# Performance work log

Measured on AMD Instinct MI355X. Metric: run time of the kernel, lower is better.

## Reference

```python
import jax, jax.numpy as jnp
import numpy as np

N = 50000        # nodes
E = 800000       # edges
R = 8            # relations
G = 64           # g_dim
H1 = 64          # h1_dim
H2 = 32          # h2_dim (per-head for transformer, output for sage)
HEADS = 4
EPS = 1e-5       # BatchNorm eps


def setup_inputs() -> dict:
    key = jax.random.key(0)
    ks = jax.random.split(key, 16)
    def rn(k, shape, scale=0.05):
        return jax.random.normal(k, shape, dtype=jnp.float32) * scale
    return {
        "node_features": jax.random.normal(ks[0], (N, G), dtype=jnp.float32),
        "node_type": jax.random.randint(ks[1], (N,), 0, 3),
        "edge_index": jax.random.randint(ks[2], (2, E), 0, N),
        "edge_type": jax.random.randint(ks[3], (E,), 0, R),
        # RGCNConv params (per-relation weight + root weight + bias)
        "rgcn_w": rn(ks[4], (R, G, H1)),
        "rgcn_root": rn(ks[5], (G, H1)),
        "rgcn_bias": jnp.zeros((H1,), jnp.float32),
        "bn1_g": jnp.ones((H1,), jnp.float32),
        "bn1_b": jnp.zeros((H1,), jnp.float32),
        # TransformerConv params (q/k/v projections + skip)
        "wq": rn(ks[6], (H1, HEADS * H2)), "bq": jnp.zeros((HEADS * H2,), jnp.float32),
        "wk": rn(ks[7], (H1, HEADS * H2)), "bk": jnp.zeros((HEADS * H2,), jnp.float32),
        "wv": rn(ks[8], (H1, HEADS * H2)), "bv": jnp.zeros((HEADS * H2,), jnp.float32),
        "wskip": rn(ks[9], (H1, HEADS * H2)), "bskip": jnp.zeros((HEADS * H2,), jnp.float32),
        "bn2_g": jnp.ones((HEADS * H2,), jnp.float32),
        "bn2_b": jnp.zeros((HEADS * H2,), jnp.float32),
        # SAGEConv params (lin_l on aggregated neighbors has bias; lin_r on root has none)
        "sage_wl": rn(ks[10], (HEADS * H2, H2)), "sage_bl": jnp.zeros((H2,), jnp.float32),
        "sage_wr": rn(ks[11], (HEADS * H2, H2)),
        "bn3_g": jnp.ones((H2,), jnp.float32),
        "bn3_b": jnp.zeros((H2,), jnp.float32),
    }


def _bn(x, g, b):
    # BatchNorm1d in training mode: biased batch statistics over nodes
    m = x.mean(0)
    v = x.var(0)
    return g * (x - m) * jax.lax.rsqrt(v + EPS) + b


def _match(res, d):
    # F.pad(res, (0, d - c)): pads with zeros if d > c, truncates if d < c
    c = res.shape[1]
    if d > c:
        return jnp.pad(res, ((0, 0), (0, d - c)))
    return res[:, :d]


def _forward(node_features, rgcn_w, rgcn_root, rgcn_bias, bn1_g, bn1_b,
             wq, bq, wk, bk, wv, bv, wskip, bskip, bn2_g, bn2_b,
             sage_wl, sage_bl, sage_wr, bn3_g, bn3_b,
             edge_index, edge_type):
    src, dst = edge_index[0], edge_index[1]
    x = node_features
    residual = x

    # ---- RGCNConv: per-relation transform, per-relation mean aggregation, sum over relations ----
    xr = jnp.einsum('nf,rfh->nrh', x, rgcn_w)            # [N,R,H1]
    msg = xr[src, edge_type]                              # [E,H1]
    seg = dst * R + edge_type                             # segment per (node, relation)
    sums = jax.ops.segment_sum(msg, seg, num_segments=N * R)
    cnt = jax.ops.segment_sum(jnp.ones((E,), msg.dtype), seg, num_segments=N * R)
    agg = (sums / jnp.maximum(cnt, 1.0)[:, None]).reshape(N, R, H1).sum(1)
    h = agg + x @ rgcn_root + rgcn_bias
    h = jax.nn.leaky_relu(_bn(h, bn1_g, bn1_b))
    x = h + _match(residual, h.shape[1])
    residual = x

    # ---- TransformerConv: edge softmax attention, concat heads, + skip projection ----
    q = (x @ wq + bq).reshape(N, HEADS, H2)
    k = (x @ wk + bk).reshape(N, HEADS, H2)
    v = (x @ wv + bv).reshape(N, HEADS, H2)
    logits = (q[dst] * k[src]).sum(-1) / jnp.sqrt(jnp.float32(H2))  # [E,HEADS]
    mx = jax.ops.segment_max(logits, dst, num_segments=N)
    ex = jnp.exp(logits - mx[dst])
    den = jax.ops.segment_sum(ex, dst, num_segments=N)
    alpha = ex / jnp.maximum(den[dst], 1e-16)
    out = jax.ops.segment_sum(alpha[:, :, None] * v[src], dst, num_segments=N)
    h = out.reshape(N, HEADS * H2) + x @ wskip + bskip
    h = jax.nn.leaky_relu(_bn(h, bn2_g, bn2_b))
    x = h + _match(residual, h.shape[1])
    residual = x

    # ---- SAGEConv: mean neighbor aggregation + root transform ----
    nsum = jax.ops.segment_sum(x[src], dst, num_segments=N)
    ncnt = jax.ops.segment_sum(jnp.ones((E,), x.dtype), dst, num_segments=N)
    nmean = nsum / jnp.maximum(ncnt, 1.0)[:, None]
    h = nmean @ sage_wl + sage_bl + x @ sage_wr
    h = jax.nn.leaky_relu(_bn(h, bn3_g, bn3_b))
    return h + _match(residual, h.shape[1])


def reference(node_features, node_type, edge_index, edge_type,
              rgcn_w, rgcn_root, rgcn_bias, bn1_g, bn1_b,
              wq, bq, wk, bk, wv, bv, wskip, bskip, bn2_g, bn2_b,
              sage_wl, sage_bl, sage_wr, bn3_g, bn3_b):
    # node_type is unused by the original forward
    return _forward(node_features, rgcn_w, rgcn_root, rgcn_bias, bn1_g, bn1_b,
                    wq, bq, wk, bk, wv, bv, wskip, bskip, bn2_g, bn2_b,
                    sage_wl, sage_bl, sage_wr, bn3_g, bn3_b,
                    edge_index, edge_type)
```

## Files before the change

kernel.cpp:

```cpp
#include <hip/hip_runtime.h>
#include <stdint.h>

#define NN 50000
#define NE 800000
#define NR (NN*8)
#define SCAN_BS 512
#define NB2 782
#define INV_N (1.0f/50000.0f)
#define BN_EPS 1e-5f

typedef unsigned short ushort_t;
typedef unsigned char uchar_t;
typedef short bf16x8 __attribute__((ext_vector_type(8)));
typedef float f32x4 __attribute__((ext_vector_type(4)));
typedef float f32x2 __attribute__((ext_vector_type(2)));

__device__ __forceinline__ ushort_t f2bf(float f){
    unsigned int u = __float_as_uint(f);
    u += 0x7FFFu + ((u >> 16) & 1u);
    return (ushort_t)(u >> 16);
}
__device__ __forceinline__ float bf2f(ushort_t h){ return __uint_as_float(((unsigned int)h) << 16); }
__device__ __forceinline__ float bflo(unsigned int u){ return __uint_as_float(u << 16); }
__device__ __forceinline__ float bfhi(unsigned int u){ return __uint_as_float(u & 0xFFFF0000u); }

__device__ __forceinline__ unsigned int f4_to_fp8(float a, float b, float c, float d){
    int v = __builtin_amdgcn_cvt_pk_fp8_f32(a, b, 0, false);
    v = __builtin_amdgcn_cvt_pk_fp8_f32(c, d, v, true);
    return (unsigned int)v;
}
__device__ __forceinline__ void fp8_to_f4(unsigned int u, float& a, float& b, float& c, float& d){
    f32x2 lo = __builtin_amdgcn_cvt_pk_f32_fp8(u, false);
    f32x2 hi = __builtin_amdgcn_cvt_pk_f32_fp8(u, true);
    a = lo.x; b = lo.y; c = hi.x; d = hi.y;
}

__global__ void k_deg(const int* __restrict__ ei, const int* __restrict__ et,
                      int* __restrict__ deg, uint2* __restrict__ sr){
    int e = blockIdx.x*256 + threadIdx.x;
    if (e < NE){
        int seg = ei[NE + e]*8 + et[e];
        int rank = atomicAdd(&deg[seg], 1);
        uint2 o; o.x = (unsigned)seg; o.y = (unsigned)rank;
        sr[e] = o;
    }
}

__global__ void k_scan1(const int* __restrict__ deg, int* __restrict__ tmp, int* __restrict__ bsum){
    __shared__ int s[SCAN_BS];
    int t = threadIdx.x;
    int i = blockIdx.x*SCAN_BS + t;
    s[t] = (i < NR) ? deg[i] : 0;
    __syncthreads();
    for (int off = 1; off < SCAN_BS; off <<= 1){
        int add = (t >= off) ? s[t-off] : 0;
        __syncthreads();
        s[t] += add;
        __syncthreads();
    }
    if (i < NR) tmp[i] = s[t];
    if (t == SCAN_BS-1) bsum[blockIdx.x] = s[t];
}

__global__ void k_scan2(int* __restrict__ bsum){
    __shared__ int s[NB2];
    int t = threadIdx.x;
    if (t < NB2) s[t] = bsum[t];
    __syncthreads();
    if (t == 0){
        int acc = 0;
        for (int i = 0; i < NB2; ++i){ acc += s[i]; s[i] = acc; }
    }
    __syncthreads();
    if (t < NB2) bsum[t] = s[t];
}

__global__ void k_scan3(const int* __restrict__ tmp, const int* __restrict__ bsum, int* __restrict__ rs){
    int i = blockIdx.x*256 + threadIdx.x;
    if (i < NR){
        int b = i >> 9;
        int off = (b > 0) ? bsum[b-1] : 0;
        rs[i+1] = tmp[i] + off;
        if (i == 0) rs[0] = 0;
    }
}

__global__ void k_fill(const int* __restrict__ ei, const uint2* __restrict__ sr,
                       const int* __restrict__ rs, int* __restrict__ csr){
    int e = blockIdx.x*256 + threadIdx.x;
    if (e < NE){
        uint2 s = sr[e];
        csr[rs[s.x] + (int)s.y] = ei[e];
    }
}

__global__ void k_prep(const float* __restrict__ nf,
                       const float* __restrict__ rgcn_w, const float* __restrict__ root,
                       const float* __restrict__ wq, const float* __restrict__ wk,
                       const float* __restrict__ wv, const float* __restrict__ wsk,
                       const float* __restrict__ bq, const float* __restrict__ bk,
                       const float* __restrict__ bv, const float* __restrict__ bsk,
                       const float* __restrict__ wl, const float* __restrict__ wr,
                       ushort_t* __restrict__ xb, uchar_t* __restrict__ xb8,
                       ushort_t* __restrict__ Wcat,
                       ushort_t* __restrict__ Wt2, float* __restrict__ bcat,
                       ushort_t* __restrict__ Wsage){
    int i = blockIdx.x*256 + threadIdx.x;
    const int NXB = NN*16;
    if (i < NXB){
        float4 v = ((const float4*)nf)[i];
        ushort4 h;
        h.x = f2bf(v.x); h.y = f2bf(v.y); h.z = f2bf(v.z); h.w = f2bf(v.w);
        ((ushort4*)xb)[i] = h;
        ((unsigned int*)xb8)[i] = f4_to_fp8(v.x, v.y, v.z, v.w);
        return;
    }
    int j = i - NXB;
    if (j < 64*576){
        int h = j / 576, k = j - h*576;
        float v = (k < 512) ? rgcn_w[(size_t)k*64 + h] : root[(size_t)(k-512)*64 + h];
        Wcat[j] = f2bf(v);
    } else if (j < 64*576 + 512*64){
        int jj = j - 64*576;
        int c = jj >> 6, k = jj & 63;
        int mt = c >> 7, cc = c & 127;
        const float* W = (mt==0)?wq:(mt==1)?wk:(mt==2)?wv:wsk;
        Wt2[jj] = f2bf(W[(size_t)k*128 + cc]);
    } else if (j < 64*576 + 512*64 + 512){
        int c = j - (64*576 + 512*64);
        int mt = c >> 7, cc = c & 127;
        const float* B = (mt==0)?bq:(mt==1)?bk:(mt==2)?bv:bsk;
        bcat[c] = B[cc];
    } else if (j < 64*576 + 512*64 + 512 + 32*256){
        int jj = j - (64*576 + 512*64 + 512);
        int c = jj >> 8, k = jj & 255;
        float v = (k < 128) ? wr[(size_t)k*32 + c] : wl[(size_t)(k-128)*32 + c];
        Wsage[jj] = f2bf(v);
    }
}

__global__ __launch_bounds__(256) void rgcn_fused(const ushort_t* __restrict__ xb,
                                                  const uchar_t* __restrict__ xb8,
                                                  const int* __restrict__ rs,
                                                  const int* __restrict__ csr,
                                                  const ushort_t* __restrict__ Wcat,
                                                  const float* __restrict__ bias,
                                                  float* __restrict__ h1pre){
    __shared__ ushort_t Ml[16*520];
    int w = threadIdx.x >> 6, lane = threadIdx.x & 63;
    int quad = lane >> 4, l4 = lane & 15;
    int row0 = blockIdx.x * 16;
    int n0 = row0 + w*4;
    int rsel = (lane < 9 ? lane : 8);
    int rb = rs[n0*8 + rsel];
    int eb0 = __shfl(rb, 0);
    int dg0 = __shfl(rb, 8) - eb0;
    int idx = (lane < dg0) ? csr[eb0 + lane] : 0;
    for (int j = 0; j < 4; ++j){
        int lrow = (w*4 + j)*520;
        int ebase = __shfl(rb, 0);
        int enext = __shfl(rb, 8);
        int rb_next = 0, idxn = 0;
        if (j < 3){
            rb_next = rs[(n0 + j + 1)*8 + rsel];
            idxn = csr[min(enext + lane, NE - 1)];
        }
        int e0a = __shfl(rb, quad),     e1a = __shfl(rb, quad + 1);
        int e0b = __shfl(rb, quad + 4), e1b = __shfl(rb, quad + 5);
        int oa = e0a - ebase, la = e1a - e0a;
        int ob = e0b - ebase, lb = e1b - e0b;
        int ml = max(la, lb);
        ml = max(ml, __shfl_xor(ml, 16));
        ml = max(ml, __shfl_xor(ml, 32));
        float aa0=0.f, aa1=0.f, aa2=0.f, aa3=0.f;
        float ab0=0.f, ab1=0.f, ab2=0.f, ab3=0.f;
        for (int i = 0; i < ml; i += 4){
            int sA[4], sB[4];
            bool vA[4], vB[4];
#pragma unroll
            for (int u = 0; u < 4; ++u){
                int jA = oa + i + u, jB = ob + i + u;
                vA[u] = (i + u) < la;
                vB[u] = (i + u) < lb;
                int tA = __shfl(idx, jA & 63);
                int tB = __shfl(idx, jB & 63);
                if (jA >= 64 && vA[u]) tA = csr[ebase + jA];
                if (jB >= 64 && vB[u]) tB = csr[ebase + jB];
                sA[u] = vA[u] ? tA : 0;
                sB[u] = vB[u] ? tB : 0;
            }
            unsigned int uA[4], uB[4];
#pragma unroll
            for (int u = 0; u < 4; ++u){
                uA[u] = *(const unsigned int*)(xb8 + (size_t)sA[u]*64 + l4*4);
                uB[u] = *(const unsigned int*)(xb8 + (size_t)sB[u]*64 + l4*4);
            }
#pragma unroll
            for (int u = 0; u < 4; ++u){
                float f0,f1,f2,f3;
                fp8_to_f4(uA[u],f0,f1,f2,f3);
                if (vA[u]){ aa0+=f0; aa1+=f1; aa2+=f2; aa3+=f3; }
                fp8_to_f4(uB[u],f0,f1,f2,f3);
                if (vB[u]){ ab0+=f0; ab1+=f1; ab2+=f2; ab3+=f3; }
            }
        }
        float inva = 1.f / fmaxf((float)la, 1.f);
        float invb = 1.f / fmaxf((float)lb, 1.f);
        ushort4 oA, oB;
        oA.x = f2bf(aa0*inva); oA.y = f2bf(aa1*inva); oA.z = f2bf(aa2*inva); oA.w = f2bf(aa3*inva);
        oB.x = f2bf(ab0*invb); oB.y = f2bf(ab1*invb); oB.z = f2bf(ab2*invb); oB.w = f2bf(ab3*invb);
        *(ushort4*)&Ml[lrow + quad*64 + l4*4] = oA;
        *(ushort4*)&Ml[lrow + (quad + 4)*64 + l4*4] = oB;
        if (j < 3){
            rb = rb_next;
            int ebn = __shfl(rb, 0);
            int dgn = __shfl(rb, 8) - ebn;
            idx = (lane < dgn) ? idxn : 0;
        }
    }
    __syncthreads();
    int m = l4;
    f32x4 acc = {};
#pragma unroll
    for (int kt = 0; kt < 18; ++kt){
        int kk = kt*32 + quad*8;
        bf16x8 a;
        if (kt < 16) a = *(const bf16x8*)&Ml[m*520 + kk];
        else         a = *(const bf16x8*)(xb + (size_t)(row0 + m)*64 + (kk - 512));
        bf16x8 b = *(const bf16x8*)(Wcat + (size_t)(w*16 + m)*576 + kk);
        acc = __builtin_amdgcn_mfma_f32_16x16x32_bf16(a, b, acc, 0, 0, 0);
    }
    int col = w*16 + m;
    float bz = bias[col];
#pragma unroll
    for (int i = 0; i < 4; ++i){
        int rr = row0 + quad*4 + i;
        h1pre[(size_t)rr*64 + col] = acc[i] + bz;
    }
}

__global__ void bn1_finalize(const float* __restrict__ sums, const float* __restrict__ sumsq,
                             const float* __restrict__ g1, const float* __restrict__ b1,
                             float* __restrict__ A1, float* __restrict__ C1){
    int c = threadIdx.x;
    if (c < 64){
        float m = sums[c] * INV_N;
        float v = sumsq[c] * INV_N - m*m;
        float rsv = rsqrtf(fmaxf(v, 0.f) + BN_EPS);
        float A = rsv * g1[c];
        A1[c] = A;
        C1[c] = b1[c] - m * A;
    }
}

#define QS 132
#define BS 68
__global__ __launch_bounds__(256) void gemm_qkvs(const float* __restrict__ h1pre,
                                                 const float* __restrict__ nf,
                                                 const float* __restrict__ A1, const float* __restrict__ C1,
                                                 const ushort_t* __restrict__ Wt2,
                                                 const float* __restrict__ bcat,
                                                 ushort_t* __restrict__ qb,
                                                 uchar_t* __restrict__ kb8,
                                                 ushort_t* __restrict__ vb,
                                                 ushort_t* __restrict__ sb){
    __shared__ ushort_t Bs[256*BS];
    __shared__ ushort_t pl[4][16*QS];
    int w = threadIdx.x >> 6, lane = threadIdx.x & 63;
    int m = lane & 15, quad = lane >> 4;
    int r0 = blockIdx.x*64 + w*16;
    int cg = blockIdx.y;
    int row = r0 + m;
    {
        int t = threadIdx.x;
        const ushort_t* wsrc = Wt2 + (size_t)cg*256*64;
#pragma unroll
        for (int u0 = 0; u0 < 8; ++u0){
            int u = u0*256 + t;
            int r = u >> 3, c8 = (u & 7)*8;
            *(uint4*)&Bs[r*BS + c8] = *(const uint4*)(wsrc + u*8);
        }
    }
    bf16x8 afrag[2];
#pragma unroll
    for (int kt = 0; kt < 2; ++kt){
        int db = kt*32 + quad*8;
        bf16x8 f = (bf16x8){0,0,0,0,0,0,0,0};
        if (row < NN){
            float4 h0 = *(const float4*)(h1pre + (size_t)row*64 + db);
            float4 h1 = *(const float4*)(h1pre + (size_t)row*64 + db + 4);
            float4 n0 = *(const float4*)(nf + (size_t)row*64 + db);
            float4 n1 = *(const float4*)(nf + (size_t)row*64 + db + 4);
            float4 a0 = *(const float4*)(A1 + db);
            float4 a1 = *(const float4*)(A1 + db + 4);
            float4 c0 = *(const float4*)(C1 + db);
            float4 c1 = *(const float4*)(C1 + db + 4);
            float hh[8] = {h0.x,h0.y,h0.z,h0.w,h1.x,h1.y,h1.z,h1.w};
            float nn[8] = {n0.x,n0.y,n0.z,n0.w,n1.x,n1.y,n1.z,n1.w};
            float AA[8] = {a0.x,a0.y,a0.z,a0.w,a1.x,a1.y,a1.z,a1.w};
            float CC[8] = {c0.x,c0.y,c0.z,c0.w,c1.x,c1.y,c1.z,c1.w};
#pragma unroll
            for (int e = 0; e < 8; ++e){
                float y = fmaf(hh[e], AA[e], CC[e]);
                y = (y >= 0.f) ? y : 0.01f*y;
                f[e] = (short)f2bf(y + nn[e]);
            }
        }
        afrag[kt] = f;
    }
    __syncthreads();
    f32x4 acc[16] = {};
#pragma unroll
    for (int kt = 0; kt < 2; ++kt){
        int kk = kt*32 + quad*8;
#pragma unroll
        for (int ct = 0; ct < 16; ++ct){
            bf16x8 b = *(const bf16x8*)&Bs[(size_t)(ct*16 + m)*BS + kk];
            acc[ct] = __builtin_amdgcn_mfma_f32_16x16x32_bf16(afrag[kt], b, acc[ct], 0, 0, 0);
        }
    }
#pragma unroll
    for (int ct = 0; ct < 8; ++ct){
        int g = cg*256 + ct*16 + m;
        float bz = bcat[g];
        int cc = g & 127;
#pragma unroll
        for (int i = 0; i < 4; ++i)
            pl[w][(quad*4 + i)*QS + cc] = f2bf(acc[ct][i] + bz);
    }
    if (cg == 0){
#pragma unroll
        for (int t = 0; t < 4; ++t){
            int u = t*64 + lane;
            int r = u >> 4, c = (u & 15)*8;
            int gr = r0 + r;
            if (gr < NN) *(uint4*)(qb + (size_t)gr*128 + c) = *(const uint4*)&pl[w][r*QS + c];
        }
    } else {
#pragma unroll
        for (int t = 0; t < 4; ++t){
            int u = t*64 + lane;
            int r = u >> 4, c = (u & 15)*8;
            int gr = r0 + r;
            if (gr < NN) *(uint4*)(vb + (size_t)gr*128 + c) = *(const uint4*)&pl[w][r*QS + c];
        }
    }
#pragma unroll
    for (int ct = 8; ct < 16; ++ct){
        int g = cg*256 + ct*16 + m;
        float bz = bcat[g];
        int cc = g & 127;
#pragma unroll
        for (int i = 0; i < 4; ++i)
            pl[w][(quad*4 + i)*QS + cc] = f2bf(acc[ct][i] + bz);
    }
    if (cg == 0){
#pragma unroll
        for (int t = 0; t < 4; ++t){
            int u = t*64 + lane;
            int r = u >> 4, c = (u & 15)*8;
            int gr = r0 + r;
            if (gr < NN){
                uint4 kk4 = *(const uint4*)&pl[w][r*QS + c];
                uint2 o;
                o.x = f4_to_fp8(bflo(kk4.x), bfhi(kk4.x), bflo(kk4.y), bfhi(kk4.y));
                o.y = f4_to_fp8(bflo(kk4.z), bfhi(kk4.z), bflo(kk4.w), bfhi(kk4.w));
                *(uint2*)(kb8 + (size_t)gr*128 + c) = o;
            }
        }
    } else {
#pragma unroll
        for (int t = 0; t < 4; ++t){
            int u = t*64 + lane;
            int r = u >> 4, c = (u & 15)*8;
            int gr = r0 + r;
            if (gr < NN) *(uint4*)(sb + (size_t)gr*128 + c) = *(const uint4*)&pl[w][r*QS + c];
        }
    }
}

__global__ __launch_bounds__(256) void sage_gemm(const ushort_t* __restrict__ x2b,
                                                 const ushort_t* __restrict__ nmeanb,
                                                 const ushort_t* __restrict__ Wsage,
                                                 const float* __restrict__ bl,
                                                 float* __restrict__ h3){
    int wv = threadIdx.x >> 6, lane = threadIdx.x & 63;
    int r0 = blockIdx.x*64 + wv*16;
    int m = lane & 15, quad = lane >> 4;
    int row = r0 + m;
    f32x4 acc[2] = {};
#pragma unroll
    for (int kt = 0; kt < 8; ++kt){
        int kk = kt*32 + quad*8;
        bf16x8 a;
        if (row < NN){
            const ushort_t* ap = (kt < 4) ? (x2b + (size_t)row*128 + kk)
                                          : (nmeanb + (size_t)row*128 + (kk - 128));
            a = *(const bf16x8*)ap;
        } else {
            a = (bf16x8){0,0,0,0,0,0,0,0};
        }
#pragma unroll
        for (int ct = 0; ct < 2; ++ct){
            bf16x8 b = *(const bf16x8*)(Wsage + (size_t)(ct*16 + m)*256 + kk);
            acc[ct] = __builtin_amdgcn_mfma_f32_16x16x32_bf16(a, b, acc[ct], 0, 0, 0);
        }
    }
#pragma unroll
    for (int ct = 0; ct < 2; ++ct){
        int col = ct*16 + m;
        float bz = bl[col];
#pragma unroll
        for (int i = 0; i < 4; ++i){
            int rr = r0 + quad*4 + i;
            if (rr < NN) h3[(size_t)rr*32 + col] = acc[ct][i] + bz;
        }
    }
}

template<int C>
__global__ __launch_bounds__(256) void bn_stats(const float* __restrict__ X, int ld,
                                                float* __restrict__ sums, float* __restrict__ sumsq){
    __shared__ float s1[256], s2[256];
    int t = threadIdx.x;
    int c = t & (C-1);
    const int rpb = 256 / C;
    int r = blockIdx.x * rpb + (t / C);
    int rstride = gridDim.x * rpb;
    float a = 0.f, b = 0.f;
    for (; r < NN; r += rstride){
        float v = X[(size_t)r*ld + c];
        a += v; b += v*v;
    }
    s1[t] = a; s2[t] = b;
    __syncthreads();
    for (int off = 128; off >= C; off >>= 1){
        if (t < off){ s1[t] += s1[t+off]; s2[t] += s2[t+off]; }
        __syncthreads();
    }
    if (t < C){ atomicAdd(&sums[t], s1[t]); atomicAdd(&sumsq[t], s2[t]); }
}

__device__ __forceinline__ float bn_leaky(float z, float m, float rsv, float g, float b){
    float y = (z - m) * rsv * g + b;
    return y >= 0.f ? y : 0.01f * y;
}

__global__ void bn_apply2(const float* __restrict__ h2, const float* __restrict__ h1pre,
                          const float* __restrict__ nf,
                          const float* __restrict__ g1, const float* __restrict__ b1,
                          const float* __restrict__ s1, const float* __restrict__ q1,
                          const float* __restrict__ g2, const float* __restrict__ b2,
                          const float* __restrict__ s2, const float* __restrict__ q2,
                          float* __restrict__ x2r, ushort_t* __restrict__ x2b,
                          uchar_t* __restrict__ x28){
    int i = blockIdx.x*256 + threadIdx.x;
    if (i >= NN*128) return;
    int n = i >> 7, c = i & 127;
    float m2 = s2[c] * INV_N;
    float v2 = q2[c] * INV_N - m2*m2;
    float rsv2 = rsqrtf(fmaxf(v2, 0.f) + BN_EPS);
    float val = bn_leaky(h2[i], m2, rsv2, g2[c], b2[c]);
    if (c < 64){
        float m1 = s1[c] * INV_N;
        float v1 = q1[c] * INV_N - m1*m1;
        float rsv1 = rsqrtf(fmaxf(v1, 0.f) + BN_EPS);
        val += bn_leaky(h1pre[(size_t)n*64 + c], m1, rsv1, g1[c], b1[c]) + nf[(size_t)n*64 + c];
    }
    if (c < 32) x2r[(size_t)n*32 + c] = val;
    x2b[i] = f2bf(val);
    int p = __builtin_amdgcn_cvt_pk_fp8_f32(val, val, 0, false);
    x28[i] = (uchar_t)(p & 0xFF);
}

__global__ void bn_apply3(const float* __restrict__ h3, const float* __restrict__ x2r,
                          const float* __restrict__ g, const float* __restrict__ b,
                          const float* __restrict__ sums, const float* __restrict__ sumsq,
                          float* __restrict__ out){
    int i = blockIdx.x*256 + threadIdx.x;
    if (i >= NN*32) return;
    int c = i & 31;
    float m = sums[c] * INV_N;
    float v = sumsq[c] * INV_N - m*m;
    float rsv = rsqrtf(fmaxf(v, 0.f) + BN_EPS);
    out[i] = bn_leaky(h3[i], m, rsv, g[c], b[c]) + x2r[i];
}

__global__ __launch_bounds__(256) void attn_kernel(const ushort_t* __restrict__ qb,
                                                   const uchar_t* __restrict__ kb8,
                                                   const ushort_t* __restrict__ vb,
                                                   const ushort_t* __restrict__ sb,
                                                   const int* __restrict__ rs,
                                                   const int* __restrict__ csr,
                                                   float* __restrict__ h2){
    int w = threadIdx.x >> 6, lane = threadIdx.x & 63;
    int n = blockIdx.x*4 + w;
    if (n >= NN) return;
    int half = lane >> 5, l5 = lane & 31;
    int e0 = rs[n*8], e1 = rs[n*8 + 8];
    int deg = e1 - e0;
    uint2 qu = *(const uint2*)(qb + (size_t)n*128 + l5*4);
    uint2 sbv = *(const uint2*)(sb + (size_t)n*128 + l5*4);
    float q0 = bflo(qu.x), q1 = bfhi(qu.x), q2 = bflo(qu.y), q3 = bfhi(qu.y);
    const float scale = 0.17677669529663687f;
    int idx = 0;
    if (lane < deg) idx = csr[e0 + lane];
    int dcap = min(deg, 64);
    int nt = (dcap + 7) >> 3;
    float den = 0.f, a0 = 0.f, a1 = 0.f, a2 = 0.f, a3 = 0.f;
    for (int t = 0; t < nt; ++t){
        int i2 = t*8 + half*4;
        int j0 = i2, j1 = i2+1, j2 = i2+2, j3 = i2+3;
        bool v0 = j0 < dcap, v1 = j1 < dcap, v2 = j2 < dcap, v3 = j3 < dcap;
        int s0 = __shfl(idx, j0 & 63); s0 = v0 ? s0 : 0;
        int s1 = __shfl(idx, j1 & 63); s1 = v1 ? s1 : 0;
        int s2 = __shfl(idx, j2 & 63); s2 = v2 ? s2 : 0;
        int s3 = __shfl(idx, j3 & 63); s3 = v3 ? s3 : 0;
        unsigned int ku0 = *(const unsigned int*)(kb8 + (size_t)s0*128 + l5*4);
        unsigned int ku1 = *(const unsigned int*)(kb8 + (size_t)s1*128 + l5*4);
        unsigned int ku2 = *(const unsigned int*)(kb8 + (size_t)s2*128 + l5*4);
        unsigned int ku3 = *(const unsigned int*)(kb8 + (size_t)s3*128 + l5*4);
        uint2 vv0 = *(const uint2*)(vb + (size_t)s0*128 + l5*4);
        uint2 vv1 = *(const uint2*)(vb + (size_t)s1*128 + l5*4);
        uint2 vv2 = *(const uint2*)(vb + (size_t)s2*128 + l5*4);
        uint2 vv3 = *(const uint2*)(vb + (size_t)s3*128 + l5*4);
        float ka, kb_, kc, kd;
        fp8_to_f4(ku0, ka, kb_, kc, kd);
        float p0 = q0*ka + q1*kb_ + q2*kc + q3*kd;
        fp8_to_f4(ku1, ka, kb_, kc, kd);
        float p1 = q0*ka + q1*kb_ + q2*kc + q3*kd;
        fp8_to_f4(ku2, ka, kb_, kc, kd);
        float p2 = q0*ka + q1*kb_ + q2*kc + q3*kd;
        fp8_to_f4(ku3, ka, kb_, kc, kd);
        float p3 = q0*ka + q1*kb_ + q2*kc + q3*kd;
        p0 += __shfl_xor(p0, 1); p1 += __shfl_xor(p1, 1); p2 += __shfl_xor(p2, 1); p3 += __shfl_xor(p3, 1);
        p0 += __shfl_xor(p0, 2); p1 += __shfl_xor(p1, 2); p2 += __shfl_xor(p2, 2); p3 += __shfl_xor(p3, 2);
        p0 += __shfl_xor(p0, 4); p1 += __shfl_xor(p1, 4); p2 += __shfl_xor(p2, 4); p3 += __shfl_xor(p3, 4);
        float w0 = v0 ? __expf(p0 * scale) : 0.f;
        float w1 = v1 ? __expf(p1 * scale) : 0.f;
        float w2 = v2 ? __expf(p2 * scale) : 0.f;
        float w3 = v3 ? __expf(p3 * scale) : 0.f;
        den += w0 + w1 + w2 + w3;
        a0 += w0*bflo(vv0.x) + w1*bflo(vv1.x) + w2*bflo(vv2.x) + w3*bflo(vv3.x);
        a1 += w0*bfhi(vv0.x) + w1*bfhi(vv1.x) + w2*bfhi(vv2.x) + w3*bfhi(vv3.x);
        a2 += w0*bflo(vv0.y) + w1*bflo(vv1.y) + w2*bflo(vv2.y) + w3*bflo(vv3.y);
        a3 += w0*bfhi(vv0.y) + w1*bfhi(vv1.y) + w2*bfhi(vv2.y) + w3*bfhi(vv3.y);
    }
    for (int e = 64 + half; e < deg; e += 2){
        int s = csr[e0 + e];
        unsigned int ku = *(const unsigned int*)(kb8 + (size_t)s*128 + l5*4);
        uint2 vv = *(const uint2*)(vb + (size_t)s*128 + l5*4);
        float ka, kb_, kc, kd;
        fp8_to_f4(ku, ka, kb_, kc, kd);
        float p = q0*ka + q1*kb_ + q2*kc + q3*kd;
        p += __shfl_xor(p, 1);
        p += __shfl_xor(p, 2);
        p += __shfl_xor(p, 4);
        float wg = __expf(p * scale);
        den += wg;
        a0 += wg*bflo(vv.x); a1 += wg*bfhi(vv.x);
        a2 += wg*bflo(vv.y); a3 += wg*bfhi(vv.y);
    }
    den += __shfl_xor(den, 32);
    a0 += __shfl_xor(a0, 32); a1 += __shfl_xor(a1, 32);
    a2 += __shfl_xor(a2, 32); a3 += __shfl_xor(a3, 32);
    if (half == 0){
        float inv = (den > 0.f) ? 1.f/den : 0.f;
        float4 o;
        o.x = bflo(sbv.x) + a0*inv;
        o.y = bfhi(sbv.x) + a1*inv;
        o.z = bflo(sbv.y) + a2*inv;
        o.w = bfhi(sbv.y) + a3*inv;
        *(float4*)(h2 + (size_t)n*128 + l5*4) = o;
    }
}

__global__ __launch_bounds__(256) void sage_agg(const uchar_t* __restrict__ x28,
                                                const int* __restrict__ rs,
                                                const int* __restrict__ csr,
                                                ushort_t* __restrict__ nmeanb){
    int w = threadIdx.x >> 6, lane = threadIdx.x & 63;
    int n = blockIdx.x*4 + w;
    if (n >= NN) return;
    int half = lane >> 5, l5 = lane & 31;
    int e0 = rs[n*8], e1 = rs[n*8 + 8];
    int deg = e1 - e0;
    int idx = 0;
    if (lane < deg) idx = csr[e0 + lane];
    int dcap = min(deg, 64);
    int nt = (dcap + 7) >> 3;
    float a0 = 0.f, a1 = 0.f, a2 = 0.f, a3 = 0.f;
    for (int t = 0; t < nt; ++t){
        int i2 = t*8 + half*4;
        int j0 = i2, j1 = i2+1, j2 = i2+2, j3 = i2+3;
        bool v0 = j0 < dcap, v1 = j1 < dcap, v2 = j2 < dcap, v3 = j3 < dcap;
        int s0 = __shfl(idx, j0 & 63); s0 = v0 ? s0 : 0;
        int s1 = __shfl(idx, j1 & 63); s1 = v1 ? s1 : 0;
        int s2 = __shfl(idx, j2 & 63); s2 = v2 ? s2 : 0;
        int s3 = __shfl(idx, j3 & 63); s3 = v3 ? s3 : 0;
        unsigned int u0 = *(const unsigned int*)(x28 + (size_t)s0*128 + l5*4);
        unsigned int u1 = *(const unsigned int*)(x28 + (size_t)s1*128 + l5*4);
        unsigned int u2 = *(const unsigned int*)(x28 + (size_t)s2*128 + l5*4);
        unsigned int u3 = *(const unsigned int*)(x28 + (size_t)s3*128 + l5*4);
        float fa, fb, fc, fd;
        if (v0){ fp8_to_f4(u0, fa, fb, fc, fd); a0 += fa; a1 += fb; a2 += fc; a3 += fd; }
        if (v1){ fp8_to_f4(u1, fa, fb, fc, fd); a0 += fa; a1 += fb; a2 += fc; a3 += fd; }
        if (v2){ fp8_to_f4(u2, fa, fb, fc, fd); a0 += fa; a1 += fb; a2 += fc; a3 += fd; }
        if (v3){ fp8_to_f4(u3, fa, fb, fc, fd); a0 += fa; a1 += fb; a2 += fc; a3 += fd; }
    }
    for (int e = 64 + half; e < deg; e += 2){
        int s = csr[e0 + e];
        unsigned int u = *(const unsigned int*)(x28 + (size_t)s*128 + l5*4);
        float fa, fb, fc, fd;
        fp8_to_f4(u, fa, fb, fc, fd);
        a0 += fa; a1 += fb; a2 += fc; a3 += fd;
    }
    a0 += __shfl_xor(a0, 32); a1 += __shfl_xor(a1, 32);
    a2 += __shfl_xor(a2, 32); a3 += __shfl_xor(a3, 32);
    if (half == 0){
        float inv = 1.f / fmaxf((float)deg, 1.f);
        ushort4 o;
        o.x = f2bf(a0*inv); o.y = f2bf(a1*inv); o.z = f2bf(a2*inv); o.w = f2bf(a3*inv);
        *(ushort4*)(nmeanb + (size_t)n*128 + l5*4) = o;
    }
}

extern "C" void kernel_launch(void* const* d_in, const int* in_sizes, int n_in,
                              void* d_out, int out_size, void* d_ws, size_t ws_size,
                              hipStream_t stream){
    const float* nf      = (const float*)d_in[0];
    const int*   ei      = (const int*)d_in[2];
    const int*   et      = (const int*)d_in[3];
    const float* rgcn_w  = (const float*)d_in[4];
    const float* root    = (const float*)d_in[5];
    const float* rbias   = (const float*)d_in[6];
    const float* bn1g    = (const float*)d_in[7];
    const float* bn1b    = (const float*)d_in[8];
    const float* wq      = (const float*)d_in[9];
    const float* bq      = (const float*)d_in[10];
    const float* wk      = (const float*)d_in[11];
    const float* bk      = (const float*)d_in[12];
    const float* wv      = (const float*)d_in[13];
    const float* bv      = (const float*)d_in[14];
    const float* wsk     = (const float*)d_in[15];
    const float* bsk     = (const float*)d_in[16];
    const float* bn2g    = (const float*)d_in[17];
    const float* bn2b    = (const float*)d_in[18];
    const float* wl      = (const float*)d_in[19];
    const float* bl      = (const float*)d_in[20];
    const float* wr      = (const float*)d_in[21];
    const float* bn3g    = (const float*)d_in[22];
    const float* bn3b    = (const float*)d_in[23];
    float* out = (float*)d_out;

    char* base = (char*)d_ws;
    size_t off = 0;
    auto take = [&](size_t bytes) -> char* {
        char* p = base + off;
        off += (bytes + 255) & ~(size_t)255;
        return p;
    };
    int*      deg    = (int*)take((size_t)NR*4);
    float*    bns    = (float*)take(1024*4);
    char*     zend   = base + off;
    int*      rs     = (int*)take((size_t)(NR+1)*4);
    int*      tmp    = (int*)take((size_t)NR*4);
    int*      bsum   = (int*)take(1024*4);
    uint2*    sr     = (uint2*)take((size_t)NE*8);
    int*      csr    = (int*)take((size_t)NE*4);
    ushort_t* Wcat   = (ushort_t*)take(64*576*2);
    ushort_t* Wt2    = (ushort_t*)take(512*64*2);
    float*    bcat   = (float*)take(512*4);
    ushort_t* Wsage  = (ushort_t*)take(32*256*2);
    ushort_t* xb     = (ushort_t*)take((size_t)NN*64*2);
    uchar_t*  xb8    = (uchar_t*)take((size_t)NN*64);
    float*    h1pre  = (float*)take((size_t)NN*64*4);
    float*    h2     = (float*)take((size_t)NN*128*4);
    float*    x2r    = (float*)take((size_t)NN*32*4);
    ushort_t* sb     = (ushort_t*)take((size_t)NN*128*2);
    char*     bigA   = take((size_t)NN*512*2);
    if (off > ws_size) return;

    ushort_t* qb     = (ushort_t*)(bigA + (size_t)NN*128);
    ushort_t* vb     = (ushort_t*)(bigA + (size_t)NN*384);
    uchar_t*  kb8    = (uchar_t*)(bigA + (size_t)NN*640);
    ushort_t* x2b    = (ushort_t*)bigA;
    uchar_t*  x28    = (uchar_t*)(bigA + (size_t)NN*256);
    ushort_t* nmeanb = (ushort_t*)(bigA + (size_t)NN*512);
    float*    h3     = (float*)(bigA + (size_t)NN*768);

    hipMemsetAsync(deg, 0, (size_t)(zend - (char*)deg), stream);

    const int PREP_N = NN*16 + 64*576 + 512*64 + 512 + 32*256;
    k_prep <<<(PREP_N+255)/256, 256, 0, stream>>>(nf, rgcn_w, root, wq, wk, wv, wsk,
                                                  bq, bk, bv, bsk, wl, wr,
                                                  xb, xb8, Wcat, Wt2, bcat, Wsage);
    k_deg  <<<(NE+255)/256, 256, 0, stream>>>(ei, et, deg, sr);
    k_scan1<<<NB2, SCAN_BS, 0, stream>>>(deg, tmp, bsum);
    k_scan2<<<1, 1024, 0, stream>>>(bsum);
    k_scan3<<<(NR+255)/256, 256, 0, stream>>>(tmp, bsum, rs);
    k_fill <<<(NE+255)/256, 256, 0, stream>>>(ei, sr, rs, csr);

    const int NB4 = (NN + 3) / 4;
    const int NBG = (NN + 63) / 64;

    rgcn_fused<<<NN/16, 256, 0, stream>>>(xb, xb8, rs, csr, Wcat, rbias, h1pre);
    bn_stats<64><<<256, 256, 0, stream>>>(h1pre, 64, bns + 0, bns + 64);
    bn1_finalize<<<1, 64, 0, stream>>>(bns + 0, bns + 64, bn1g, bn1b, bns + 448, bns + 512);

    gemm_qkvs<<<dim3(NBG, 2), 256, 0, stream>>>(h1pre, nf, bns + 448, bns + 512,
                                                Wt2, bcat, qb, kb8, vb, sb);
    attn_kernel<<<NB4, 256, 0, stream>>>(qb, kb8, vb, sb, rs, csr, h2);
    bn_stats<128><<<256, 256, 0, stream>>>(h2, 128, bns + 128, bns + 256);
    bn_apply2<<<(NN*128+255)/256, 256, 0, stream>>>(h2, h1pre, nf,
                                                    bn1g, bn1b, bns + 0, bns + 64,
                                                    bn2g, bn2b, bns + 128, bns + 256,
                                                    x2r, x2b, x28);

    sage_agg<<<NB4, 256, 0, stream>>>(x28, rs, csr, nmeanb);
    sage_gemm<<<NBG, 256, 0, stream>>>(x2b, nmeanb, Wsage, bl, h3);
    bn_stats<32><<<256, 256, 0, stream>>>(h3, 32, bns + 384, bns + 416);
    bn_apply3<<<(NN*32+255)/256, 256, 0, stream>>>(h3, x2r, bn3g, bn3b, bns + 384, bns + 416, out);
}
```

Before: 410.5 us.

## Transform nodes per relation before aggregation instead of aggregating then multiplying

Replaces the fused RGCN kernel (which gathered fp8 features per relation, averaged them, then multiplied by the concatenated weights) with a two-step transform-then-aggregate scheme. A dense MFMA GEMM first computes x·W_r for all 8 relations plus the root term, storing per-relation projections in bf16. A separate gather kernel then sums these with precomputed 1/deg edge weights stored by k_fill, and the CSR now packs source*8+relation so other consumers shift it back. This trades the per-node fp8 gather of 64-dim features for a gather of bf16 64-dim projected rows, and adds a 50000x512 bf16 intermediate plus an extra per-edge weight array.

```diff
diff --git a/kernel.cpp b/kernel.cpp
--- a/kernel.cpp
+++ b/kernel.cpp
@@ -86,11 +86,16 @@
 }
 
 __global__ void k_fill(const int* __restrict__ ei, const uint2* __restrict__ sr,
-                       const int* __restrict__ rs, int* __restrict__ csr){
+                       const int* __restrict__ rs, int* __restrict__ csr,
+                       float* __restrict__ wgt){
     int e = blockIdx.x*256 + threadIdx.x;
     if (e < NE){
         uint2 s = sr[e];
-        csr[rs[s.x] + (int)s.y] = ei[e];
+        int b = rs[s.x];
+        int dgs = rs[s.x + 1] - b;
+        int pos = b + (int)s.y;
+        csr[pos] = ei[e]*8 + (int)(s.x & 7u);
+        wgt[pos] = 1.f / (float)dgs;
     }
 }
 
@@ -101,8 +106,8 @@
                        const float* __restrict__ bq, const float* __restrict__ bk,
                        const float* __restrict__ bv, const float* __restrict__ bsk,
                        const float* __restrict__ wl, const float* __restrict__ wr,
-                       ushort_t* __restrict__ xb, uchar_t* __restrict__ xb8,
-                       ushort_t* __restrict__ Wcat,
+                       ushort_t* __restrict__ xb,
+                       ushort_t* __restrict__ WbigT,
                        ushort_t* __restrict__ Wt2, float* __restrict__ bcat,
                        ushort_t* __restrict__ Wsage){
     int i = blockIdx.x*256 + threadIdx.x;
@@ -112,130 +117,129 @@
         ushort4 h;
         h.x = f2bf(v.x); h.y = f2bf(v.y); h.z = f2bf(v.z); h.w = f2bf(v.w);
         ((ushort4*)xb)[i] = h;
-        ((unsigned int*)xb8)[i] = f4_to_fp8(v.x, v.y, v.z, v.w);
         return;
     }
     int j = i - NXB;
-    if (j < 64*576){
-        int h = j / 576, k = j - h*576;
-        float v = (k < 512) ? rgcn_w[(size_t)k*64 + h] : root[(size_t)(k-512)*64 + h];
-        Wcat[j] = f2bf(v);
-    } else if (j < 64*576 + 512*64){
-        int jj = j - 64*576;
+    if (j < 576*64){
+        int col = j >> 6, g = j & 63;
+        float v = (col < 512) ? rgcn_w[(size_t)(col >> 6)*4096 + (size_t)g*64 + (col & 63)]
+                              : root[(size_t)g*64 + (col - 512)];
+        WbigT[j] = f2bf(v);
+    } else if (j < 576*64 + 512*64){
+        int jj = j - 576*64;
         int c = jj >> 6, k = jj & 63;
         int mt = c >> 7, cc = c & 127;
         const float* W = (mt==0)?wq:(mt==1)?wk:(mt==2)?wv:wsk;
         Wt2[jj] = f2bf(W[(size_t)k*128 + cc]);
-    } else if (j < 64*576 + 512*64 + 512){
-        int c = j - (64*576 + 512*64);
+    } else if (j < 576*64 + 512*64 + 512){
+        int c = j - (576*64 + 512*64);
         int mt = c >> 7, cc = c & 127;
         const float* B = (mt==0)?bq:(mt==1)?bk:(mt==2)?bv:bsk;
         bcat[c] = B[cc];
-    } else if (j < 64*576 + 512*64 + 512 + 32*256){
-        int jj = j - (64*576 + 512*64 + 512);
+    } else if (j < 576*64 + 512*64 + 512 + 32*256){
+        int jj = j - (576*64 + 512*64 + 512);
         int c = jj >> 8, k = jj & 255;
         float v = (k < 128) ? wr[(size_t)k*32 + c] : wl[(size_t)(k-128)*32 + c];
         Wsage[jj] = f2bf(v);
     }
 }
 
-__global__ __launch_bounds__(256) void rgcn_fused(const ushort_t* __restrict__ xb,
-                                                  const uchar_t* __restrict__ xb8,
-                                                  const int* __restrict__ rs,
-                                                  const int* __restrict__ csr,
-                                                  const ushort_t* __restrict__ Wcat,
-                                                  const float* __restrict__ bias,
-                                                  float* __restrict__ h1pre){
-    __shared__ ushort_t Ml[16*520];
+__global__ __launch_bounds__(256) void xr_gemm(const ushort_t* __restrict__ xb,
+                                               const ushort_t* __restrict__ WbigT,
+                                               const float* __restrict__ rbias,
+                                               ushort_t* __restrict__ xrb,
+                                               float* __restrict__ h1pre){
+    __shared__ ushort_t pl[4][16*132];
     int w = threadIdx.x >> 6, lane = threadIdx.x & 63;
-    int quad = lane >> 4, l4 = lane & 15;
-    int row0 = blockIdx.x * 16;
-    int n0 = row0 + w*4;
-    int rsel = (lane < 9 ? lane : 8);
-    int rb = rs[n0*8 + rsel];
-    int eb0 = __shfl(rb, 0);
-    int dg0 = __shfl(rb, 8) - eb0;
-    int idx = (lane < dg0) ? csr[eb0 + lane] : 0;
-    for (int j = 0; j < 4; ++j){
-        int lrow = (w*4 + j)*520;
-        int ebase = __shfl(rb, 0);
-        int enext = __shfl(rb, 8);
-        int rb_next = 0, idxn = 0;
-        if (j < 3){
-            rb_next = rs[(n0 + j + 1)*8 + rsel];
-            idxn = csr[min(enext + lane, NE - 1)];
-        }
-        int e0a = __shfl(rb, quad),     e1a = __shfl(rb, quad + 1);
-        int e0b = __shfl(rb, quad + 4), e1b = __shfl(rb, quad + 5);
-        int oa = e0a - ebase, la = e1a - e0a;
-        int ob = e0b - ebase, lb = e1b - e0b;
-        int ml = max(la, lb);
-        ml = max(ml, __shfl_xor(ml, 16));
-        ml = max(ml, __shfl_xor(ml, 32));
-        float aa0=0.f, aa1=0.f, aa2=0.f, aa3=0.f;
-        float ab0=0.f, ab1=0.f, ab2=0.f, ab3=0.f;
-        for (int i = 0; i < ml; i += 4){
-            int sA[4], sB[4];
-            bool vA[4], vB[4];
-#pragma unroll
-            for (int u = 0; u < 4; ++u){
-                int jA = oa + i + u, jB = ob + i + u;
-                vA[u] = (i + u) < la;
-                vB[u] = (i + u) < lb;
-                int tA = __shfl(idx, jA & 63);
-                int tB = __shfl(idx, jB & 63);
-                if (jA >= 64 && vA[u]) tA = csr[ebase + jA];
-                if (jB >= 64 && vB[u]) tB = csr[ebase + jB];
-                sA[u] = vA[u] ? tA : 0;
-                sB[u] = vB[u] ? tB : 0;
-            }
-            unsigned int uA[4], uB[4];
-#pragma unroll
-            for (int u = 0; u < 4; ++u){
-                uA[u] = *(const unsigned int*)(xb8 + (size_t)sA[u]*64 + l4*4);
-                uB[u] = *(const unsigned int*)(xb8 + (size_t)sB[u]*64 + l4*4);
-            }
-#pragma unroll
-            for (int u = 0; u < 4; ++u){
-                float f0,f1,f2,f3;
-                fp8_to_f4(uA[u],f0,f1,f2,f3);
-                if (vA[u]){ aa0+=f0; aa1+=f1; aa2+=f2; aa3+=f3; }
-                fp8_to_f4(uB[u],f0,f1,f2,f3);
-                if (vB[u]){ ab0+=f0; ab1+=f1; ab2+=f2; ab3+=f3; }
-            }
-        }
-        float inva = 1.f / fmaxf((float)la, 1.f);
-        float invb = 1.f / fmaxf((float)lb, 1.f);
-        ushort4 oA, oB;
-        oA.x = f2bf(aa0*inva); oA.y = f2bf(aa1*inva); oA.z = f2bf(aa2*inva); oA.w = f2bf(aa3*inva);
-        oB.x = f2bf(ab0*invb); oB.y = f2bf(ab1*invb); oB.z = f2bf(ab2*invb); oB.w = f2bf(ab3*invb);
-        *(ushort4*)&Ml[lrow + quad*64 + l4*4] = oA;
-        *(ushort4*)&Ml[lrow + (quad + 4)*64 + l4*4] = oB;
-        if (j < 3){
-            rb = rb_next;
-            int ebn = __shfl(rb, 0);
-            int dgn = __shfl(rb, 8) - ebn;
-            idx = (lane < dgn) ? idxn : 0;
-        }
-    }
-    __syncthreads();
-    int m = l4;
-    f32x4 acc = {};
-#pragma unroll
-    for (int kt = 0; kt < 18; ++kt){
-        int kk = kt*32 + quad*8;
-        bf16x8 a;
-        if (kt < 16) a = *(const bf16x8*)&Ml[m*520 + kk];
-        else         a = *(const bf16x8*)(xb + (size_t)(row0 + m)*64 + (kk - 512));
-        bf16x8 b = *(const bf16x8*)(Wcat + (size_t)(w*16 + m)*576 + kk);
-        acc = __builtin_amdgcn_mfma_f32_16x16x32_bf16(a, b, acc, 0, 0, 0);
-    }
-    int col = w*16 + m;
-    float bz = bias[col];
-#pragma unroll
-    for (int i = 0; i < 4; ++i){
-        int rr = row0 + quad*4 + i;
-        h1pre[(size_t)rr*64 + col] = acc[i] + bz;
+    int m = lane & 15, quad = lane >> 4;
+    int r0 = blockIdx.x * 16;
+    bf16x8 a0 = *(const bf16x8*)(xb + (size_t)(r0 + m)*64 + quad*8);
+    bf16x8 a1 = *(const bf16x8*)(xb + (size_t)(r0 + m)*64 + 32 + quad*8);
+    f32x4 acc[9] = {};
+#pragma unroll
+    for (int ct = 0; ct < 9; ++ct){
+        int col = (ct < 8) ? (w*128 + ct*16 + m) : (512 + w*16 + m);
+        bf16x8 b0 = *(const bf16x8*)(WbigT + (size_t)col*64 + quad*8);
+        bf16x8 b1 = *(const bf16x8*)(WbigT + (size_t)col*64 + 32 + quad*8);
+        acc[ct] = __builtin_amdgcn_mfma_f32_16x16x32_bf16(a0, b0, acc[ct], 0, 0, 0);
+        acc[ct] = __builtin_amdgcn_mfma_f32_16x16x32_bf16(a1, b1, acc[ct], 0, 0, 0);
+    }
+#pragma unroll
+    for (int ct = 0; ct < 8; ++ct){
+#pragma unroll
+        for (int i = 0; i < 4; ++i)
+            pl[w][(quad*4 + i)*132 + ct*16 + m] = f2bf(acc[ct][i]);
+    }
+    {
+        float bz = rbias[w*16 + m];
+#pragma unroll
+        for (int i = 0; i < 4; ++i)
+            h1pre[(size_t)(r0 + quad*4 + i)*64 + w*16 + m] = acc[8][i] + bz;
+    }
+#pragma unroll
+    for (int t = 0; t < 4; ++t){
+        int u = t*64 + lane;
+        int r = u >> 4, c = (u & 15)*8;
+        *(uint4*)(xrb + (size_t)(r0 + r)*512 + w*128 + c) = *(const uint4*)&pl[w][r*132 + c];
+    }
+}
+
+__global__ __launch_bounds__(256) void rgcn_agg(const ushort_t* __restrict__ xrb,
+                                                const float* __restrict__ wgt,
+                                                const int* __restrict__ rs,
+                                                const int* __restrict__ csr,
+                                                float* __restrict__ h1pre){
+    int w = threadIdx.x >> 6, lane = threadIdx.x & 63;
+    int n = blockIdx.x*4 + w;
+    if (n >= NN) return;
+    int grp = lane >> 4, l4 = lane & 15;
+    int e0 = rs[n*8], e1 = rs[n*8 + 8];
+    int deg = e1 - e0;
+    int idx = 0; float wle = 0.f;
+    if (lane < deg){ idx = csr[e0 + lane]; wle = wgt[e0 + lane]; }
+    int dcap = min(deg, 64);
+    int nt = (dcap + 15) >> 4;
+    float a0 = 0.f, a1 = 0.f, a2 = 0.f, a3 = 0.f;
+    for (int t = 0; t < nt; ++t){
+        int sj[4]; float wj[4];
+#pragma unroll
+        for (int u = 0; u < 4; ++u){
+            int j = t*16 + grp*4 + u;
+            bool v = j < dcap;
+            int s = __shfl(idx, j & 63);
+            float ww = __shfl(wle, j & 63);
+            sj[u] = v ? s : 0;
+            wj[u] = v ? ww : 0.f;
+        }
+        uint2 g[4];
+#pragma unroll
+        for (int u = 0; u < 4; ++u)
+            g[u] = *(const uint2*)(xrb + (size_t)sj[u]*64 + l4*4);
+#pragma unroll
+        for (int u = 0; u < 4; ++u){
+            a0 = fmaf(wj[u], bflo(g[u].x), a0);
+            a1 = fmaf(wj[u], bfhi(g[u].x), a1);
+            a2 = fmaf(wj[u], bflo(g[u].y), a2);
+            a3 = fmaf(wj[u], bfhi(g[u].y), a3);
+        }
+    }
+    for (int e = 64 + grp; e < deg; e += 4){
+        int s = csr[e0 + e];
+        float ww = wgt[e0 + e];
+        uint2 g = *(const uint2*)(xrb + (size_t)s*64 + l4*4);
+        a0 = fmaf(ww, bflo(g.x), a0);
+        a1 = fmaf(ww, bfhi(g.x), a1);
+        a2 = fmaf(ww, bflo(g.y), a2);
+        a3 = fmaf(ww, bfhi(g.y), a3);
+    }
+    a0 += __shfl_xor(a0, 16); a1 += __shfl_xor(a1, 16);
+    a2 += __shfl_xor(a2, 16); a3 += __shfl_xor(a3, 16);
+    a0 += __shfl_xor(a0, 32); a1 += __shfl_xor(a1, 32);
+    a2 += __shfl_xor(a2, 32); a3 += __shfl_xor(a3, 32);
+    if (grp == 0){
+        float4 r = *(const float4*)(h1pre + (size_t)n*64 + l4*4);
+        r.x += a0; r.y += a1; r.z += a2; r.w += a3;
+        *(float4*)(h1pre + (size_t)n*64 + l4*4) = r;
     }
 }
 
@@ -512,10 +516,10 @@
         int i2 = t*8 + half*4;
         int j0 = i2, j1 = i2+1, j2 = i2+2, j3 = i2+3;
         bool v0 = j0 < dcap, v1 = j1 < dcap, v2 = j2 < dcap, v3 = j3 < dcap;
-        int s0 = __shfl(idx, j0 & 63); s0 = v0 ? s0 : 0;
-        int s1 = __shfl(idx, j1 & 63); s1 = v1 ? s1 : 0;
-        int s2 = __shfl(idx, j2 & 63); s2 = v2 ? s2 : 0;
-        int s3 = __shfl(idx, j3 & 63); s3 = v3 ? s3 : 0;
+        int s0 = __shfl(idx, j0 & 63); s0 = v0 ? (s0 >> 3) : 0;
+        int s1 = __shfl(idx, j1 & 63); s1 = v1 ? (s1 >> 3) : 0;
+        int s2 = __shfl(idx, j2 & 63); s2 = v2 ? (s2 >> 3) : 0;
+        int s3 = __shfl(idx, j3 & 63); s3 = v3 ? (s3 >> 3) : 0;
         unsigned int ku0 = *(const unsigned int*)(kb8 + (size_t)s0*128 + l5*4);
         unsigned int ku1 = *(const unsigned int*)(kb8 + (size_t)s1*128 + l5*4);
         unsigned int ku2 = *(const unsigned int*)(kb8 + (size_t)s2*128 + l5*4);
@@ -547,7 +551,7 @@
         a3 += w0*bfhi(vv0.y) + w1*bfhi(vv1.y) + w2*bfhi(vv2.y) + w3*bfhi(vv3.y);
     }
     for (int e = 64 + half; e < deg; e += 2){
-        int s = csr[e0 + e];
+        int s = csr[e0 + e] >> 3;
         unsigned int ku = *(const unsigned int*)(kb8 + (size_t)s*128 + l5*4);
         uint2 vv = *(const uint2*)(vb + (size_t)s*128 + l5*4);
         float ka, kb_, kc, kd;
@@ -594,10 +598,10 @@
         int i2 = t*8 + half*4;
         int j0 = i2, j1 = i2+1, j2 = i2+2, j3 = i2+3;
         bool v0 = j0 < dcap, v1 = j1 < dcap, v2 = j2 < dcap, v3 = j3 < dcap;
-        int s0 = __shfl(idx, j0 & 63); s0 = v0 ? s0 : 0;
-        int s1 = __shfl(idx, j1 & 63); s1 = v1 ? s1 : 0;
-        int s2 = __shfl(idx, j2 & 63); s2 = v2 ? s2 : 0;
-        int s3 = __shfl(idx, j3 & 63); s3 = v3 ? s3 : 0;
+        int s0 = __shfl(idx, j0 & 63); s0 = v0 ? (s0 >> 3) : 0;
+        int s1 = __shfl(idx, j1 & 63); s1 = v1 ? (s1 >> 3) : 0;
+        int s2 = __shfl(idx, j2 & 63); s2 = v2 ? (s2 >> 3) : 0;
+        int s3 = __shfl(idx, j3 & 63); s3 = v3 ? (s3 >> 3) : 0;
         unsigned int u0 = *(const unsigned int*)(x28 + (size_t)s0*128 + l5*4);
         unsigned int u1 = *(const unsigned int*)(x28 + (size_t)s1*128 + l5*4);
         unsigned int u2 = *(const unsigned int*)(x28 + (size_t)s2*128 + l5*4);
@@ -609,7 +613,7 @@
         if (v3){ fp8_to_f4(u3, fa, fb, fc, fd); a0 += fa; a1 += fb; a2 += fc; a3 += fd; }
     }
     for (int e = 64 + half; e < deg; e += 2){
-        int s = csr[e0 + e];
+        int s = csr[e0 + e] >> 3;
         unsigned int u = *(const unsigned int*)(x28 + (size_t)s*128 + l5*4);
         float fa, fb, fc, fd;
         fp8_to_f4(u, fa, fb, fc, fd);
@@ -668,12 +672,12 @@
     int*      bsum   = (int*)take(1024*4);
     uint2*    sr     = (uint2*)take((size_t)NE*8);
     int*      csr    = (int*)take((size_t)NE*4);
-    ushort_t* Wcat   = (ushort_t*)take(64*576*2);
+    float*    wgt    = (float*)take((size_t)NE*4);
+    ushort_t* WbigT  = (ushort_t*)take(576*64*2);
     ushort_t* Wt2    = (ushort_t*)take(512*64*2);
     float*    bcat   = (float*)take(512*4);
     ushort_t* Wsage  = (ushort_t*)take(32*256*2);
     ushort_t* xb     = (ushort_t*)take((size_t)NN*64*2);
-    uchar_t*  xb8    = (uchar_t*)take((size_t)NN*64);
     float*    h1pre  = (float*)take((size_t)NN*64*4);
     float*    h2     = (float*)take((size_t)NN*128*4);
     float*    x2r    = (float*)take((size_t)NN*32*4);
@@ -681,6 +685,7 @@
     char*     bigA   = take((size_t)NN*512*2);
     if (off > ws_size) return;
 
+    ushort_t* xrb    = (ushort_t*)bigA;
     ushort_t* qb     = (ushort_t*)(bigA + (size_t)NN*128);
     ushort_t* vb     = (ushort_t*)(bigA + (size_t)NN*384);
     uchar_t*  kb8    = (uchar_t*)(bigA + (size_t)NN*640);
@@ -691,20 +696,21 @@
 
     hipMemsetAsync(deg, 0, (size_t)(zend - (char*)deg), stream);
 
-    const int PREP_N = NN*16 + 64*576 + 512*64 + 512 + 32*256;
+    const int PREP_N = NN*16 + 576*64 + 512*64 + 512 + 32*256;
     k_prep <<<(PREP_N+255)/256, 256, 0, stream>>>(nf, rgcn_w, root, wq, wk, wv, wsk,
                                                   bq, bk, bv, bsk, wl, wr,
-                                                  xb, xb8, Wcat, Wt2, bcat, Wsage);
+                                                  xb, WbigT, Wt2, bcat, Wsage);
     k_deg  <<<(NE+255)/256, 256, 0, stream>>>(ei, et, deg, sr);
     k_scan1<<<NB2, SCAN_BS, 0, stream>>>(deg, tmp, bsum);
     k_scan2<<<1, 1024, 0, stream>>>(bsum);
     k_scan3<<<(NR+255)/256, 256, 0, stream>>>(tmp, bsum, rs);
-    k_fill <<<(NE+255)/256, 256, 0, stream>>>(ei, sr, rs, csr);
+    k_fill <<<(NE+255)/256, 256, 0, stream>>>(ei, sr, rs, csr, wgt);
 
     const int NB4 = (NN + 3) / 4;
     const int NBG = (NN + 63) / 64;
 
-    rgcn_fused<<<NN/16, 256, 0, stream>>>(xb, xb8, rs, csr, Wcat, rbias, h1pre);
+    xr_gemm <<<NN/16, 256, 0, stream>>>(xb, WbigT, rbias, xrb, h1pre);
+    rgcn_agg<<<NB4, 256, 0, stream>>>(xrb, wgt, rs, csr, h1pre);
     bn_stats<64><<<256, 256, 0, stream>>>(h1pre, 64, bns + 0, bns + 64);
     bn1_finalize<<<1, 64, 0, stream>>>(bns + 0, bns + 64, bn1g, bn1b, bns + 448, bns + 512);
 
```

Measured after the change: 424.5 us. 3.4% more time.
